# Performance work log

Hardware: AMD Instinct MI355X
Metric: run time of the kernel (lower is better)

The kernel has to match this reference:

```python
import jax, jax.numpy as jnp
import numpy as np

N_HEAD = 16
WINDOW = 256


def setup_inputs() -> dict:
    key = jax.random.key(0)
    ks = jax.random.split(key, 3)
    B, S, D = 2, 2048, 1024
    x = jax.random.normal(ks[0], (B, S, D), dtype=jnp.float32)
    w_attn = jax.random.normal(ks[1], (D, 3 * D), dtype=jnp.float32) * 0.02
    b_attn = jnp.zeros((3 * D,), dtype=jnp.float32)
    w_proj = jax.random.normal(ks[2], (D, D), dtype=jnp.float32) * 0.02
    b_proj = jnp.zeros((D,), dtype=jnp.float32)
    return {"x": x, "w_attn": w_attn, "b_attn": b_attn, "w_proj": w_proj, "b_proj": b_proj}


def reference(x, w_attn, b_attn, w_proj, b_proj):
    B, S, D = x.shape
    hd = D // N_HEAD  # head dim
    scale = 1.0 / np.sqrt(hd).astype(np.float32)

    # fused QKV projection (Conv1D == linear on last dim)
    c = jnp.einsum('bsd,df->bsf', x, w_attn) + b_attn
    q, k, v = jnp.split(c, 3, axis=-1)

    def split_heads(t):  # [B,S,D] -> [B,H,S,hd]
        return t.reshape(B, S, N_HEAD, hd).transpose(0, 2, 1, 3)

    q, k, v = split_heads(q), split_heads(k), split_heads(v)
    present = jnp.stack([k, v], axis=1)  # [B,2,H,S,hd]

    # scores [B,H,S,S]
    w = jnp.einsum('bhqd,bhkd->bhqk', q, k) * scale

    # causal sliding-window mask
    q_pos = jnp.arange(S)[:, None]
    k_pos = jnp.arange(S)[None, :]
    mask = (k_pos <= q_pos) & (k_pos >= q_pos - WINDOW + 1)  # [S,S]
    w = jnp.where(mask[None, None], w, jnp.finfo(w.dtype).min)
    w = jax.nn.softmax(w, axis=-1)

    a = jnp.einsum('bhqk,bhkd->bhqd', w, v)
    a = a.transpose(0, 2, 1, 3).reshape(B, S, D)  # merge heads
    out = jnp.einsum('bsd,df->bsf', a, w_proj) + b_proj
    return out, present
```

## Files before the change

kernel.cpp:

```cpp
#include <hip/hip_runtime.h>
#include <cstdint>
#include <cstddef>

typedef __bf16 bf16x8 __attribute__((ext_vector_type(8)));
typedef float f32x4 __attribute__((ext_vector_type(4)));

#define MFMA16(a, b, c) __builtin_amdgcn_mfma_f32_16x16x32_bf16(a, b, c, 0, 0, 0)

static __device__ __forceinline__ bf16x8 ld_bf16x8(const __bf16* p) {
    return *reinterpret_cast<const bf16x8*>(p);
}

static __device__ __forceinline__ void async_cp16(const __bf16* g, __bf16* l) {
    __builtin_amdgcn_global_load_lds((const __attribute__((address_space(1))) void*)g,
                                     (__attribute__((address_space(3))) void*)l, 16, 0, 0);
}

template <int N>
static __device__ __forceinline__ void wait_vmcnt() {
    asm volatile("s_waitcnt vmcnt(%0)" ::"n"(N) : "memory");
}

static __device__ __forceinline__ void barrier_pinned() {
    __builtin_amdgcn_sched_barrier(0);
    __builtin_amdgcn_s_barrier();
    __builtin_amdgcn_sched_barrier(0);
}

static __device__ __forceinline__ float ex2(float x) {
    return __builtin_amdgcn_exp2f(x);
}

template <int CTRL>
static __device__ __forceinline__ float dppmv(float x) {
    return __builtin_bit_cast(float, __builtin_amdgcn_update_dpp(
        0, __builtin_bit_cast(int, x), CTRL, 0xF, 0xF, true));
}
static __device__ __forceinline__ float rmax16(float x) {
    x = fmaxf(x, dppmv<0x121>(x));
    x = fmaxf(x, dppmv<0x122>(x));
    x = fmaxf(x, dppmv<0x124>(x));
    x = fmaxf(x, dppmv<0x128>(x));
    return x;
}
static __device__ __forceinline__ float rsum16(float x) {
    x += dppmv<0x121>(x);
    x += dppmv<0x122>(x);
    x += dppmv<0x124>(x);
    x += dppmv<0x128>(x);
    return x;
}

__global__ void cvt_kernel(const float* __restrict__ src, __bf16* __restrict__ dst, int n8) {
    int i = blockIdx.x * blockDim.x + threadIdx.x;
    if (i >= n8) return;
    const float4* s4 = reinterpret_cast<const float4*>(src) + (size_t)i * 2;
    float4 a = s4[0], b = s4[1];
    bf16x8 o;
    o[0] = (__bf16)a.x; o[1] = (__bf16)a.y; o[2] = (__bf16)a.z; o[3] = (__bf16)a.w;
    o[4] = (__bf16)b.x; o[5] = (__bf16)b.y; o[6] = (__bf16)b.z; o[7] = (__bf16)b.w;
    reinterpret_cast<bf16x8*>(dst)[i] = o;
}

__global__ __launch_bounds__(256) void tcvt_kernel(const float* __restrict__ in,
                                                   __bf16* __restrict__ out, int K, int N) {
    __shared__ __bf16 T[64][72];
    const int k0 = blockIdx.y * 64, n0 = blockIdx.x * 64;
    const int t = threadIdx.x;
    const int col = (t & 15) << 2;
    const int rowb = t >> 4;
    #pragma unroll
    for (int i = 0; i < 4; i++) {
        int row = i * 16 + rowb;
        float4 v = *reinterpret_cast<const float4*>(&in[(size_t)(k0 + row) * N + n0 + col]);
        T[col + 0][row] = (__bf16)v.x;
        T[col + 1][row] = (__bf16)v.y;
        T[col + 2][row] = (__bf16)v.z;
        T[col + 3][row] = (__bf16)v.w;
    }
    __syncthreads();
    const int oc = (t & 7) << 3;
    const int orb = t >> 3;
    #pragma unroll
    for (int i = 0; i < 2; i++) {
        int r = i * 32 + orb;
        bf16x8 v = *reinterpret_cast<bf16x8*>(&T[r][oc]);
        *reinterpret_cast<bf16x8*>(&out[(size_t)(n0 + r) * K + k0 + oc]) = v;
    }
}

template <int BM, int BN, int WM, int WN>
__device__ __forceinline__ void mainloop2(const __bf16* __restrict__ A,
                                          const __bf16* __restrict__ Bt,
                                          int K, int row0, int col0,
                                          __bf16* lds,
                                          f32x4 (&acc)[BM / WM / 16][BN / WN / 16]) {
    constexpr int MR = BM / WM / 16, NR = BN / WN / 16;
    constexpr int AE = BM * 32;
    constexpr int BUFE = AE + BN * 32;
    constexpr int APW = BM / 16 / 8;
    constexpr int BPW = BN / 16 / 8;
    const int tid = threadIdx.x, l = tid & 63, w = tid >> 6;
    const int wm = w / WN, wn = w % WN;
    const int lr = l >> 2;
    const int lcs = (((l & 3) ^ ((l >> 3) & 3)) << 3);
    const int fr = l & 15;
    const int fc = (((l >> 4) ^ ((l >> 1) & 3)) << 3);

    const size_t arow = (size_t)(row0 + lr) * K + lcs;
    const size_t brow = (size_t)(col0 + lr) * K + lcs;
    const int nt = K >> 5;

    auto stage = [&](int t, int buf) {
        const int k0 = t << 5;
        const int bb = buf * BUFE;
        #pragma unroll
        for (int j = 0; j < APW; j++) {
            const int mi = w * APW + j;
            async_cp16(A + arow + (size_t)mi * 16 * K + k0, lds + bb + mi * 512 + l * 8);
        }
        #pragma unroll
        for (int j = 0; j < BPW; j++) {
            const int ni = w * BPW + j;
            async_cp16(Bt + brow + (size_t)ni * 16 * K + k0, lds + bb + AE + ni * 512 + l * 8);
        }
    };

    stage(0, 0);
    stage(1, 1);

    const int aoff = (wm * (BM / WM) + fr) * 32 + fc;
    const int boff = AE + (wn * (BN / WN) + fr) * 32 + fc;

    int p = 0;
    for (int t = 0; t < nt; ++t) {
        if (t + 1 < nt) {
            wait_vmcnt<APW + BPW>();
        } else {
            wait_vmcnt<0>();
        }
        barrier_pinned();
        if (t + 2 < nt) {
            int p2 = p + 2; if (p2 >= 3) p2 -= 3;
            stage(t + 2, p2);
        }
        const int cb = p * BUFE;
        bf16x8 af[MR], bfv[NR];
        #pragma unroll
        for (int m = 0; m < MR; m++) af[m] = ld_bf16x8(&lds[cb + aoff + m * 512]);
        #pragma unroll
        for (int n = 0; n < NR; n++) bfv[n] = ld_bf16x8(&lds[cb + boff + n * 512]);
        __builtin_amdgcn_s_setprio(1);
        #pragma unroll
        for (int m = 0; m < MR; m++) {
            #pragma unroll
            for (int n = 0; n < NR; n++) {
                acc[m][n] = MFMA16(af[m], bfv[n], acc[m][n]);
            }
        }
        __builtin_amdgcn_s_setprio(0);
        asm volatile("s_waitcnt lgkmcnt(0)" ::: "memory");
        __builtin_amdgcn_sched_barrier(0);
        p = (p == 2) ? 0 : p + 1;
    }
}

__global__ __launch_bounds__(512, 2) void gemm_qkv_kernel(const __bf16* __restrict__ xb,
                                                          const __bf16* __restrict__ wabt,
                                                          const float* __restrict__ bias,
                                                          __bf16* __restrict__ qb,
                                                          __bf16* __restrict__ kb,
                                                          __bf16* __restrict__ vt,
                                                          float* __restrict__ present) {
    __shared__ __bf16 lds[3 * (256 * 32 + 128 * 32)];
    f32x4 acc[4][4] = {};
    const int row0 = blockIdx.y * 256, col0 = blockIdx.x * 128;
    mainloop2<256, 128, 4, 2>(xb, wabt, 1024, row0, col0, lds, acc);

    const int l = threadIdx.x & 63, w = threadIdx.x >> 6;
    const int wm = w >> 1, wn = w & 1;
    const int part = col0 >> 10;
    #pragma unroll
    for (int n = 0; n < 4; n++) {
        int col = col0 + wn * 64 + n * 16 + (l & 15);
        int hh = (col >> 6) & 15;
        int dd = col & 63;
        float bv = bias[col];
        #pragma unroll
        for (int m = 0; m < 4; m++) {
            #pragma unroll
            for (int r = 0; r < 4; r++) {
                int row = row0 + wm * 64 + m * 16 + ((l >> 4) << 2) + r;
                int bb = row >> 11, ss = row & 2047;
                float val = acc[m][n][r] + bv;
                size_t qi = (((size_t)(bb * 16 + hh)) * 2048 + ss) * 64 + dd;
                if (part == 0) {
                    qb[qi] = (__bf16)val;
                } else if (part == 1) {
                    kb[qi] = (__bf16)val;
                    present[(((size_t)((bb * 2 + 0) * 16 + hh)) * 2048 + ss) * 64 + dd] = val;
                } else {
                    vt[(((size_t)(bb * 16 + hh)) * 64 + dd) * 2048 + ss] = (__bf16)val;
                    present[(((size_t)((bb * 2 + 1) * 16 + hh)) * 2048 + ss) * 64 + dd] = val;
                }
            }
        }
    }
}

__global__ __launch_bounds__(512, 2) void gemm_proj_kernel(const __bf16* __restrict__ ab,
                                                           const __bf16* __restrict__ wpbt,
                                                           const float* __restrict__ bias,
                                                           float* __restrict__ out) {
    __shared__ __bf16 lds[3 * (128 * 32 + 128 * 32)];
    f32x4 acc[2][4] = {};
    const int row0 = blockIdx.y * 128, col0 = blockIdx.x * 128;
    mainloop2<128, 128, 4, 2>(ab, wpbt, 1024, row0, col0, lds, acc);

    const int lane = threadIdx.x & 63, w = threadIdx.x >> 6;
    const int wm = w >> 1, wn = w & 1;
    #pragma unroll
    for (int n = 0; n < 4; n++) {
        int col = col0 + wn * 64 + n * 16 + (lane & 15);
        float bv = bias[col];
        #pragma unroll
        for (int m = 0; m < 2; m++) {
            #pragma unroll
            for (int r = 0; r < 4; r++) {
                int row = row0 + wm * 32 + m * 16 + ((lane >> 4) << 2) + r;
                out[(size_t)row * 1024 + col] = acc[m][n][r] + bv;
            }
        }
    }
}

__global__ __launch_bounds__(256) void attn_kernel(const __bf16* __restrict__ qb,
                                                   const __bf16* __restrict__ kb,
                                                   const __bf16* __restrict__ vtb,
                                                   __bf16* __restrict__ ab) {
    __shared__ __bf16 Pls[4][16 * 72];
    const int bidx = blockIdx.x;
    const int xcd = bidx & 7, idx = bidx >> 3;
    const int bh = (xcd << 2) | (idx & 3);
    const int qt = idx >> 2;
    const int lane = threadIdx.x & 63, wid = threadIdx.x >> 6;
    const int q0w = qt * 64 + wid * 16;

    const __bf16* Qh = qb + (size_t)bh * 2048 * 64;
    const __bf16* Kh = kb + (size_t)bh * 2048 * 64;
    const __bf16* Vt = vtb + (size_t)bh * 64 * 2048;
    __bf16* Pw = &Pls[wid][0];

    const int ld16 = lane & 15, hi3 = (lane >> 4) << 3;

    bf16x8 qf[2];
    {
        const __bf16* qp = Qh + (size_t)(q0w + ld16) * 64 + hi3;
        qf[0] = ld_bf16x8(qp);
        qf[1] = ld_bf16x8(qp + 32);
    }

    f32x4 o[4];
    #pragma unroll
    for (int dt = 0; dt < 4; dt++) o[dt] = (f32x4){0.f, 0.f, 0.f, 0.f};
    float mrun[4] = {-1e30f, -1e30f, -1e30f, -1e30f};
    float srun[4] = {0.f, 0.f, 0.f, 0.f};

    const float cl2 = 0.18033688f;
    int klo = q0w - 255;
    int kt0 = klo > 0 ? (klo & ~63) : 0;
    const int ktend = q0w + 15;

    for (int kt = kt0; kt <= ktend; kt += 64) {
        bf16x8 kf[4][2];
        #pragma unroll
        for (int kc = 0; kc < 4; kc++) {
            const __bf16* kp = Kh + (size_t)(kt + kc * 16 + ld16) * 64 + hi3;
            kf[kc][0] = ld_bf16x8(kp);
            kf[kc][1] = ld_bf16x8(kp + 32);
        }
        bf16x8 va[4], vb[4];
        #pragma unroll
        for (int dt = 0; dt < 4; dt++) {
            const __bf16* vp = &Vt[(size_t)(dt * 16 + ld16) * 2048 + kt + hi3];
            va[dt] = ld_bf16x8(vp);
            vb[dt] = ld_bf16x8(vp + 32);
        }
        f32x4 s[4];
        __builtin_amdgcn_s_setprio(1);
        #pragma unroll
        for (int kc = 0; kc < 4; kc++) {
            f32x4 a = (f32x4){0.f, 0.f, 0.f, 0.f};
            a = MFMA16(qf[0], kf[kc][0], a);
            a = MFMA16(qf[1], kf[kc][1], a);
            s[kc] = a;
        }
        __builtin_amdgcn_s_setprio(0);
        const bool clean = (kt >= q0w - 240) && (kt + 63 <= q0w);
        float pv0[4], pv1[4], pv2[4], pv3[4];
        if (clean) {
            float mxs[4];
            #pragma unroll
            for (int r = 0; r < 4; r++) {
                float m = fmaxf(fmaxf(s[0][r], s[1][r]), fmaxf(s[2][r], s[3][r]));
                mxs[r] = rmax16(m) * cl2;
            }
            float grow = fmaxf(fmaxf(mxs[0] - mrun[0], mxs[1] - mrun[1]),
                               fmaxf(mxs[2] - mrun[2], mxs[3] - mrun[3]));
            if (__all(grow <= 8.f)) {
                #pragma unroll
                for (int r = 0; r < 4; r++) {
                    float p0 = ex2(s[0][r] * cl2 - mrun[r]);
                    float p1 = ex2(s[1][r] * cl2 - mrun[r]);
                    float p2 = ex2(s[2][r] * cl2 - mrun[r]);
                    float p3 = ex2(s[3][r] * cl2 - mrun[r]);
                    srun[r] += rsum16((p0 + p1) + (p2 + p3));
                    pv0[r] = p0; pv1[r] = p1; pv2[r] = p2; pv3[r] = p3;
                }
            } else {
                float factor[4];
                #pragma unroll
                for (int r = 0; r < 4; r++) {
                    float mn = fmaxf(mrun[r], mxs[r]);
                    float f = ex2(mrun[r] - mn);
                    float p0 = ex2(s[0][r] * cl2 - mn);
                    float p1 = ex2(s[1][r] * cl2 - mn);
                    float p2 = ex2(s[2][r] * cl2 - mn);
                    float p3 = ex2(s[3][r] * cl2 - mn);
                    srun[r] = srun[r] * f + rsum16((p0 + p1) + (p2 + p3));
                    mrun[r] = mn;
                    factor[r] = f;
                    pv0[r] = p0; pv1[r] = p1; pv2[r] = p2; pv3[r] = p3;
                }
                #pragma unroll
                for (int dt = 0; dt < 4; dt++) {
                    #pragma unroll
                    for (int r = 0; r < 4; r++) o[dt][r] *= factor[r];
                }
            }
        } else {
            float factor[4];
            #pragma unroll
            for (int r = 0; r < 4; r++) {
                int q = q0w + ((lane >> 4) << 2) + r;
                int kb0 = kt + ld16;
                bool ok0 = (kb0 <= q) && (kb0 > q - 256);
                bool ok1 = (kb0 + 16 <= q) && (kb0 + 16 > q - 256);
                bool ok2 = (kb0 + 32 <= q) && (kb0 + 32 > q - 256);
                bool ok3 = (kb0 + 48 <= q) && (kb0 + 48 > q - 256);
                float t0 = ok0 ? s[0][r] * cl2 : -1e30f;
                float t1 = ok1 ? s[1][r] * cl2 : -1e30f;
                float t2 = ok2 ? s[2][r] * cl2 : -1e30f;
                float t3 = ok3 ? s[3][r] * cl2 : -1e30f;
                float mx = rmax16(fmaxf(fmaxf(t0, t1), fmaxf(t2, t3)));
                float mn = fmaxf(mrun[r], mx);
                float f = ex2(mrun[r] - mn);
                float p0 = ok0 ? ex2(t0 - mn) : 0.f;
                float p1 = ok1 ? ex2(t1 - mn) : 0.f;
                float p2 = ok2 ? ex2(t2 - mn) : 0.f;
                float p3 = ok3 ? ex2(t3 - mn) : 0.f;
                srun[r] = srun[r] * f + rsum16((p0 + p1) + (p2 + p3));
                mrun[r] = mn;
                factor[r] = f;
                pv0[r] = p0; pv1[r] = p1; pv2[r] = p2; pv3[r] = p3;
            }
            #pragma unroll
            for (int dt = 0; dt < 4; dt++) {
                #pragma unroll
                for (int r = 0; r < 4; r++) o[dt][r] *= factor[r];
            }
        }
        #pragma unroll
        for (int r = 0; r < 4; r++) {
            int qrow = ((lane >> 4) << 2) + r;
            Pw[qrow * 72 + ld16]      = (__bf16)pv0[r];
            Pw[qrow * 72 + 16 + ld16] = (__bf16)pv1[r];
            Pw[qrow * 72 + 32 + ld16] = (__bf16)pv2[r];
            Pw[qrow * 72 + 48 + ld16] = (__bf16)pv3[r];
        }
        asm volatile("s_waitcnt lgkmcnt(0)" ::: "memory");
        bf16x8 pfA = ld_bf16x8(&Pw[ld16 * 72 + hi3]);
        bf16x8 pfB = ld_bf16x8(&Pw[ld16 * 72 + 32 + hi3]);
        __builtin_amdgcn_s_setprio(1);
        #pragma unroll
        for (int dt = 0; dt < 4; dt++) o[dt] = MFMA16(pfA, va[dt], o[dt]);
        #pragma unroll
        for (int dt = 0; dt < 4; dt++) o[dt] = MFMA16(pfB, vb[dt], o[dt]);
        __builtin_amdgcn_s_setprio(0);
    }

    const int bb = bh >> 4, hh = bh & 15;
    #pragma unroll
    for (int r = 0; r < 4; r++) {
        int q = q0w + ((lane >> 4) << 2) + r;
        float inv = 1.f / srun[r];
        size_t base = ((size_t)bb * 2048 + q) * 1024 + hh * 64;
        #pragma unroll
        for (int dt = 0; dt < 4; dt++) {
            ab[base + dt * 16 + ld16] = (__bf16)(o[dt][r] * inv);
        }
    }
}

extern "C" void kernel_launch(void* const* d_in, const int* in_sizes, int n_in,
                              void* d_out, int out_size, void* d_ws, size_t ws_size,
                              hipStream_t stream) {
    const float* x = (const float*)d_in[0];
    const float* w_attn = (const float*)d_in[1];
    const float* b_attn = (const float*)d_in[2];
    const float* w_proj = (const float*)d_in[3];
    const float* b_proj = (const float*)d_in[4];

    float* out = (float*)d_out;
    float* present = out + (size_t)2 * 2048 * 1024;

    char* w = (char*)d_ws;
    __bf16* xb   = (__bf16*)(w);
    __bf16* wabt = (__bf16*)(w + 8388608);
    __bf16* wpbt = (__bf16*)(w + 14680064);
    __bf16* qb   = (__bf16*)(w + 16777216);
    __bf16* kb   = (__bf16*)(w + 25165824);
    __bf16* vt   = (__bf16*)(w + 33554432);
    __bf16* ab   = xb;

    cvt_kernel<<<2048, 256, 0, stream>>>(x, xb, 524288);
    tcvt_kernel<<<dim3(48, 16), 256, 0, stream>>>(w_attn, wabt, 1024, 3072);
    tcvt_kernel<<<dim3(16, 16), 256, 0, stream>>>(w_proj, wpbt, 1024, 1024);

    gemm_qkv_kernel<<<dim3(24, 16), 512, 0, stream>>>(xb, wabt, b_attn, qb, kb, vt, present);

    attn_kernel<<<1024, 256, 0, stream>>>(qb, kb, vt, ab);

    gemm_proj_kernel<<<dim3(8, 32), 512, 0, stream>>>(ab, wpbt, b_proj, out);
}
```

Baseline: 125.9 us.

## Split attention key range across wave pairs and shrink QKV GEMM row tile

The attention kernel now gives each 16-query tile to two waves that process alternating 64-key blocks. Their partial softmax states are merged through shared memory, so the grid doubles to 2048 blocks and each wave runs fewer serial iterations. The QKV GEMM row tile is halved from 256 to 128, doubling its grid to raise occupancy and CU coverage across the device. The cost is an extra barrier and LDS combine step in attention, plus less operand reuse per GEMM tile.

```diff
diff --git a/kernel.cpp b/kernel.cpp
--- a/kernel.cpp
+++ b/kernel.cpp
@@ -172,10 +172,10 @@
                                                           __bf16* __restrict__ kb,
                                                           __bf16* __restrict__ vt,
                                                           float* __restrict__ present) {
-    __shared__ __bf16 lds[3 * (256 * 32 + 128 * 32)];
-    f32x4 acc[4][4] = {};
-    const int row0 = blockIdx.y * 256, col0 = blockIdx.x * 128;
-    mainloop2<256, 128, 4, 2>(xb, wabt, 1024, row0, col0, lds, acc);
+    __shared__ __bf16 lds[3 * (128 * 32 + 128 * 32)];
+    f32x4 acc[2][4] = {};
+    const int row0 = blockIdx.y * 128, col0 = blockIdx.x * 128;
+    mainloop2<128, 128, 4, 2>(xb, wabt, 1024, row0, col0, lds, acc);
 
     const int l = threadIdx.x & 63, w = threadIdx.x >> 6;
     const int wm = w >> 1, wn = w & 1;
@@ -187,10 +187,10 @@
         int dd = col & 63;
         float bv = bias[col];
         #pragma unroll
-        for (int m = 0; m < 4; m++) {
-            #pragma unroll
-            for (int r = 0; r < 4; r++) {
-                int row = row0 + wm * 64 + m * 16 + ((l >> 4) << 2) + r;
+        for (int m = 0; m < 2; m++) {
+            #pragma unroll
+            for (int r = 0; r < 4; r++) {
+                int row = row0 + wm * 32 + m * 16 + ((l >> 4) << 2) + r;
                 int bb = row >> 11, ss = row & 2047;
                 float val = acc[m][n][r] + bv;
                 size_t qi = (((size_t)(bb * 16 + hh)) * 2048 + ss) * 64 + dd;
@@ -239,19 +239,21 @@
                                                    const __bf16* __restrict__ vtb,
                                                    __bf16* __restrict__ ab) {
     __shared__ __bf16 Pls[4][16 * 72];
+    __shared__ float combsh[2176];
     const int bidx = blockIdx.x;
     const int xcd = bidx & 7, idx = bidx >> 3;
     const int bh = (xcd << 2) | (idx & 3);
     const int qt = idx >> 2;
     const int lane = threadIdx.x & 63, wid = threadIdx.x >> 6;
-    const int q0w = qt * 64 + wid * 16;
+    const int qsub = wid >> 1, half = wid & 1;
+    const int q0w = qt * 32 + qsub * 16;
 
     const __bf16* Qh = qb + (size_t)bh * 2048 * 64;
     const __bf16* Kh = kb + (size_t)bh * 2048 * 64;
     const __bf16* Vt = vtb + (size_t)bh * 64 * 2048;
     __bf16* Pw = &Pls[wid][0];
 
-    const int ld16 = lane & 15, hi3 = (lane >> 4) << 3;
+    const int ld16 = lane & 15, hi3 = (lane >> 4) << 3, hi4 = (lane >> 4) << 2;
 
     bf16x8 qf[2];
     {
@@ -271,7 +273,7 @@
     int kt0 = klo > 0 ? (klo & ~63) : 0;
     const int ktend = q0w + 15;
 
-    for (int kt = kt0; kt <= ktend; kt += 64) {
+    for (int kt = kt0 + half * 64; kt <= ktend; kt += 128) {
         bf16x8 kf[4][2];
         #pragma unroll
         for (int kc = 0; kc < 4; kc++) {
@@ -342,7 +344,7 @@
             float factor[4];
             #pragma unroll
             for (int r = 0; r < 4; r++) {
-                int q = q0w + ((lane >> 4) << 2) + r;
+                int q = q0w + hi4 + r;
                 int kb0 = kt + ld16;
                 bool ok0 = (kb0 <= q) && (kb0 > q - 256);
                 bool ok1 = (kb0 + 16 <= q) && (kb0 + 16 > q - 256);
@@ -372,7 +374,7 @@
         }
         #pragma unroll
         for (int r = 0; r < 4; r++) {
-            int qrow = ((lane >> 4) << 2) + r;
+            int qrow = hi4 + r;
             Pw[qrow * 72 + ld16]      = (__bf16)pv0[r];
             Pw[qrow * 72 + 16 + ld16] = (__bf16)pv1[r];
             Pw[qrow * 72 + 32 + ld16] = (__bf16)pv2[r];
@@ -389,15 +391,45 @@
         __builtin_amdgcn_s_setprio(0);
     }
 
-    const int bb = bh >> 4, hh = bh & 15;
-    #pragma unroll
-    for (int r = 0; r < 4; r++) {
-        int q = q0w + ((lane >> 4) << 2) + r;
-        float inv = 1.f / srun[r];
-        size_t base = ((size_t)bb * 2048 + q) * 1024 + hh * 64;
+    if (half == 1) {
         #pragma unroll
         for (int dt = 0; dt < 4; dt++) {
-            ab[base + dt * 16 + ld16] = (__bf16)(o[dt][r] * inv);
+            #pragma unroll
+            for (int r = 0; r < 4; r++) {
+                combsh[(qsub * 16 + hi4 + r) * 66 + dt * 16 + ld16] = o[dt][r];
+            }
+        }
+        if (ld16 == 0) {
+            #pragma unroll
+            for (int r = 0; r < 4; r++) {
+                combsh[2112 + qsub * 16 + hi4 + r] = mrun[r];
+                combsh[2144 + qsub * 16 + hi4 + r] = srun[r];
+            }
+        }
+    }
+    __syncthreads();
+    if (half == 0) {
+        float f0[4], f1[4];
+        #pragma unroll
+        for (int r = 0; r < 4; r++) {
+            float m1 = combsh[2112 + qsub * 16 + hi4 + r];
+            float s1 = combsh[2144 + qsub * 16 + hi4 + r];
+            float mm = fmaxf(mrun[r], m1);
+            f0[r] = ex2(mrun[r] - mm);
+            f1[r] = ex2(m1 - mm);
+            srun[r] = srun[r] * f0[r] + s1 * f1[r];
+        }
+        const int bb = bh >> 4, hh = bh & 15;
+        #pragma unroll
+        for (int r = 0; r < 4; r++) {
+            int q = q0w + hi4 + r;
+            float inv = 1.f / srun[r];
+            size_t base = ((size_t)bb * 2048 + q) * 1024 + hh * 64;
+            #pragma unroll
+            for (int dt = 0; dt < 4; dt++) {
+                float o1 = combsh[(qsub * 16 + hi4 + r) * 66 + dt * 16 + ld16];
+                ab[base + dt * 16 + ld16] = (__bf16)((o[dt][r] * f0[r] + o1 * f1[r]) * inv);
+            }
         }
     }
 }
@@ -427,9 +459,9 @@
     tcvt_kernel<<<dim3(48, 16), 256, 0, stream>>>(w_attn, wabt, 1024, 3072);
     tcvt_kernel<<<dim3(16, 16), 256, 0, stream>>>(w_proj, wpbt, 1024, 1024);
 
-    gemm_qkv_kernel<<<dim3(24, 16), 512, 0, stream>>>(xb, wabt, b_attn, qb, kb, vt, present);
-
-    attn_kernel<<<1024, 256, 0, stream>>>(qb, kb, vt, ab);
+    gemm_qkv_kernel<<<dim3(24, 32), 512, 0, stream>>>(xb, wabt, b_attn, qb, kb, vt, present);
+
+    attn_kernel<<<2048, 256, 0, stream>>>(qb, kb, vt, ab);
 
     gemm_proj_kernel<<<dim3(8, 32), 512, 0, stream>>>(ab, wpbt, b_proj, out);
 }
```

Result: faster. 120.0 us (-4.7%).

## Use two-pass softmax with LDS-staged K tiles and smaller QKV GEMM tiles

Applied to the files above, without the earlier changes.

The attention kernel now stages every K tile the block needs into swizzled LDS with async copies, then runs two passes. The first pass computes QK^T to find the exact row max. The second recomputes the scores and exponentiates against that fixed max, which removes online-softmax rescaling, per-tile cross-lane reductions and branches, at the cost of doing the QK MFMAs twice. The QKV GEMM tile shrinks from 256x128 to 128x128 and the grid doubles, giving more blocks for better CU coverage. The attention kernel also gets an occupancy hint of 3 blocks per CU.

```diff
diff --git a/kernel.cpp b/kernel.cpp
--- a/kernel.cpp
+++ b/kernel.cpp
@@ -172,10 +172,10 @@
                                                           __bf16* __restrict__ kb,
                                                           __bf16* __restrict__ vt,
                                                           float* __restrict__ present) {
-    __shared__ __bf16 lds[3 * (256 * 32 + 128 * 32)];
-    f32x4 acc[4][4] = {};
-    const int row0 = blockIdx.y * 256, col0 = blockIdx.x * 128;
-    mainloop2<256, 128, 4, 2>(xb, wabt, 1024, row0, col0, lds, acc);
+    __shared__ __bf16 lds[3 * (128 * 32 + 128 * 32)];
+    f32x4 acc[2][4] = {};
+    const int row0 = blockIdx.y * 128, col0 = blockIdx.x * 128;
+    mainloop2<128, 128, 4, 2>(xb, wabt, 1024, row0, col0, lds, acc);
 
     const int l = threadIdx.x & 63, w = threadIdx.x >> 6;
     const int wm = w >> 1, wn = w & 1;
@@ -187,10 +187,10 @@
         int dd = col & 63;
         float bv = bias[col];
         #pragma unroll
-        for (int m = 0; m < 4; m++) {
+        for (int m = 0; m < 2; m++) {
             #pragma unroll
             for (int r = 0; r < 4; r++) {
-                int row = row0 + wm * 64 + m * 16 + ((l >> 4) << 2) + r;
+                int row = row0 + wm * 32 + m * 16 + ((l >> 4) << 2) + r;
                 int bb = row >> 11, ss = row & 2047;
                 float val = acc[m][n][r] + bv;
                 size_t qi = (((size_t)(bb * 16 + hh)) * 2048 + ss) * 64 + dd;
@@ -234,24 +234,38 @@
     }
 }
 
-__global__ __launch_bounds__(256) void attn_kernel(const __bf16* __restrict__ qb,
-                                                   const __bf16* __restrict__ kb,
-                                                   const __bf16* __restrict__ vtb,
-                                                   __bf16* __restrict__ ab) {
+__global__ __launch_bounds__(256, 3) void attn_kernel(const __bf16* __restrict__ qb,
+                                                      const __bf16* __restrict__ kb,
+                                                      const __bf16* __restrict__ vtb,
+                                                      __bf16* __restrict__ ab) {
+    __shared__ __bf16 Kls[5 * 4096];
     __shared__ __bf16 Pls[4][16 * 72];
     const int bidx = blockIdx.x;
     const int xcd = bidx & 7, idx = bidx >> 3;
     const int bh = (xcd << 2) | (idx & 3);
-    const int qt = idx >> 2;
+    const int qc = idx >> 2;
     const int lane = threadIdx.x & 63, wid = threadIdx.x >> 6;
-    const int q0w = qt * 64 + wid * 16;
+    const int q0blk = qc * 64;
+    const int q0w = q0blk + wid * 16;
 
     const __bf16* Qh = qb + (size_t)bh * 2048 * 64;
     const __bf16* Kh = kb + (size_t)bh * 2048 * 64;
     const __bf16* Vt = vtb + (size_t)bh * 64 * 2048;
     __bf16* Pw = &Pls[wid][0];
 
-    const int ld16 = lane & 15, hi3 = (lane >> 4) << 3;
+    const int ld16 = lane & 15, hi3 = (lane >> 4) << 3, hi4 = (lane >> 4) << 2;
+
+    int tmp = q0blk - 255;
+    const int kt0 = tmp > 0 ? (tmp & ~63) : 0;
+    const int NT = ((q0blk + 63 - kt0) >> 6) + 1;
+
+    const int sswz = (((lane & 7) ^ (lane >> 3)) << 3);
+    for (int j = wid; j < NT * 8; j += 4) {
+        const int tj = j >> 3, c = j & 7;
+        const int kt = kt0 + tj * 64;
+        const __bf16* src = Kh + (size_t)(kt + c * 8 + (lane >> 3)) * 64 + sswz;
+        async_cp16(src, &Kls[j * 512 + lane * 8]);
+    }
 
     bf16x8 qf[2];
     {
@@ -259,26 +273,62 @@
         qf[0] = ld_bf16x8(qp);
         qf[1] = ld_bf16x8(qp + 32);
     }
+    wait_vmcnt<0>();
+    __syncthreads();
+
+    const float cl2 = 0.18033688f;
+    const int rdswz = (lane & 7) << 3;
+
+    auto qks = [&](int t, int kt, f32x4 (&s)[4]) {
+        const __bf16* tb = &Kls[t * 4096];
+        #pragma unroll
+        for (int kc = 0; kc < 4; kc++) {
+            const int rbase = (kc * 16 + ld16) * 64;
+            bf16x8 k0 = ld_bf16x8(&tb[rbase + ((hi3) ^ rdswz)]);
+            bf16x8 k1 = ld_bf16x8(&tb[rbase + ((32 + hi3) ^ rdswz)]);
+            f32x4 a = (f32x4){0.f, 0.f, 0.f, 0.f};
+            a = MFMA16(qf[0], k0, a);
+            a = MFMA16(qf[1], k1, a);
+            s[kc] = a;
+        }
+        const bool clean = (kt >= q0w - 240) && (kt + 63 <= q0w);
+        if (!clean) {
+            #pragma unroll
+            for (int r = 0; r < 4; r++) {
+                int q = q0w + hi4 + r;
+                #pragma unroll
+                for (int kc = 0; kc < 4; kc++) {
+                    int ki = kt + kc * 16 + ld16;
+                    bool ok = (ki <= q) && (ki > q - 256);
+                    s[kc][r] = ok ? s[kc][r] : -1e30f;
+                }
+            }
+        }
+    };
+
+    float mr[4] = {-1e30f, -1e30f, -1e30f, -1e30f};
+    for (int t = 0; t < NT; t++) {
+        const int kt = kt0 + t * 64;
+        if (kt + 63 < q0w - 255 || kt > q0w + 15) continue;
+        f32x4 s[4];
+        qks(t, kt, s);
+        #pragma unroll
+        for (int r = 0; r < 4; r++) {
+            mr[r] = fmaxf(mr[r], fmaxf(fmaxf(s[0][r], s[1][r]), fmaxf(s[2][r], s[3][r])));
+        }
+    }
+    float m2[4];
+    #pragma unroll
+    for (int r = 0; r < 4; r++) m2[r] = rmax16(mr[r]) * cl2;
 
     f32x4 o[4];
     #pragma unroll
     for (int dt = 0; dt < 4; dt++) o[dt] = (f32x4){0.f, 0.f, 0.f, 0.f};
-    float mrun[4] = {-1e30f, -1e30f, -1e30f, -1e30f};
-    float srun[4] = {0.f, 0.f, 0.f, 0.f};
-
-    const float cl2 = 0.18033688f;
-    int klo = q0w - 255;
-    int kt0 = klo > 0 ? (klo & ~63) : 0;
-    const int ktend = q0w + 15;
-
-    for (int kt = kt0; kt <= ktend; kt += 64) {
-        bf16x8 kf[4][2];
-        #pragma unroll
-        for (int kc = 0; kc < 4; kc++) {
-            const __bf16* kp = Kh + (size_t)(kt + kc * 16 + ld16) * 64 + hi3;
-            kf[kc][0] = ld_bf16x8(kp);
-            kf[kc][1] = ld_bf16x8(kp + 32);
-        }
+    float sl[4] = {0.f, 0.f, 0.f, 0.f};
+
+    for (int t = 0; t < NT; t++) {
+        const int kt = kt0 + t * 64;
+        if (kt + 63 < q0w - 255 || kt > q0w + 15) continue;
         bf16x8 va[4], vb[4];
         #pragma unroll
         for (int dt = 0; dt < 4; dt++) {
@@ -287,96 +337,19 @@
             vb[dt] = ld_bf16x8(vp + 32);
         }
         f32x4 s[4];
-        __builtin_amdgcn_s_setprio(1);
-        #pragma unroll
-        for (int kc = 0; kc < 4; kc++) {
-            f32x4 a = (f32x4){0.f, 0.f, 0.f, 0.f};
-            a = MFMA16(qf[0], kf[kc][0], a);
-            a = MFMA16(qf[1], kf[kc][1], a);
-            s[kc] = a;
-        }
-        __builtin_amdgcn_s_setprio(0);
-        const bool clean = (kt >= q0w - 240) && (kt + 63 <= q0w);
-        float pv0[4], pv1[4], pv2[4], pv3[4];
-        if (clean) {
-            float mxs[4];
-            #pragma unroll
-            for (int r = 0; r < 4; r++) {
-                float m = fmaxf(fmaxf(s[0][r], s[1][r]), fmaxf(s[2][r], s[3][r]));
-                mxs[r] = rmax16(m) * cl2;
-            }
-            float grow = fmaxf(fmaxf(mxs[0] - mrun[0], mxs[1] - mrun[1]),
-                               fmaxf(mxs[2] - mrun[2], mxs[3] - mrun[3]));
-            if (__all(grow <= 8.f)) {
-                #pragma unroll
-                for (int r = 0; r < 4; r++) {
-                    float p0 = ex2(s[0][r] * cl2 - mrun[r]);
-                    float p1 = ex2(s[1][r] * cl2 - mrun[r]);
-                    float p2 = ex2(s[2][r] * cl2 - mrun[r]);
-                    float p3 = ex2(s[3][r] * cl2 - mrun[r]);
-                    srun[r] += rsum16((p0 + p1) + (p2 + p3));
-                    pv0[r] = p0; pv1[r] = p1; pv2[r] = p2; pv3[r] = p3;
-                }
-            } else {
-                float factor[4];
-                #pragma unroll
-                for (int r = 0; r < 4; r++) {
-                    float mn = fmaxf(mrun[r], mxs[r]);
-                    float f = ex2(mrun[r] - mn);
-                    float p0 = ex2(s[0][r] * cl2 - mn);
-                    float p1 = ex2(s[1][r] * cl2 - mn);
-                    float p2 = ex2(s[2][r] * cl2 - mn);
-                    float p3 = ex2(s[3][r] * cl2 - mn);
-                    srun[r] = srun[r] * f + rsum16((p0 + p1) + (p2 + p3));
-                    mrun[r] = mn;
-                    factor[r] = f;
-                    pv0[r] = p0; pv1[r] = p1; pv2[r] = p2; pv3[r] = p3;
-                }
-                #pragma unroll
-                for (int dt = 0; dt < 4; dt++) {
-                    #pragma unroll
-                    for (int r = 0; r < 4; r++) o[dt][r] *= factor[r];
-                }
-            }
-        } else {
-            float factor[4];
-            #pragma unroll
-            for (int r = 0; r < 4; r++) {
-                int q = q0w + ((lane >> 4) << 2) + r;
-                int kb0 = kt + ld16;
-                bool ok0 = (kb0 <= q) && (kb0 > q - 256);
-                bool ok1 = (kb0 + 16 <= q) && (kb0 + 16 > q - 256);
-                bool ok2 = (kb0 + 32 <= q) && (kb0 + 32 > q - 256);
-                bool ok3 = (kb0 + 48 <= q) && (kb0 + 48 > q - 256);
-                float t0 = ok0 ? s[0][r] * cl2 : -1e30f;
-                float t1 = ok1 ? s[1][r] * cl2 : -1e30f;
-                float t2 = ok2 ? s[2][r] * cl2 : -1e30f;
-                float t3 = ok3 ? s[3][r] * cl2 : -1e30f;
-                float mx = rmax16(fmaxf(fmaxf(t0, t1), fmaxf(t2, t3)));
-                float mn = fmaxf(mrun[r], mx);
-                float f = ex2(mrun[r] - mn);
-                float p0 = ok0 ? ex2(t0 - mn) : 0.f;
-                float p1 = ok1 ? ex2(t1 - mn) : 0.f;
-                float p2 = ok2 ? ex2(t2 - mn) : 0.f;
-                float p3 = ok3 ? ex2(t3 - mn) : 0.f;
-                srun[r] = srun[r] * f + rsum16((p0 + p1) + (p2 + p3));
-                mrun[r] = mn;
-                factor[r] = f;
-                pv0[r] = p0; pv1[r] = p1; pv2[r] = p2; pv3[r] = p3;
-            }
-            #pragma unroll
-            for (int dt = 0; dt < 4; dt++) {
-                #pragma unroll
-                for (int r = 0; r < 4; r++) o[dt][r] *= factor[r];
-            }
-        }
+        qks(t, kt, s);
         #pragma unroll
         for (int r = 0; r < 4; r++) {
-            int qrow = ((lane >> 4) << 2) + r;
-            Pw[qrow * 72 + ld16]      = (__bf16)pv0[r];
-            Pw[qrow * 72 + 16 + ld16] = (__bf16)pv1[r];
-            Pw[qrow * 72 + 32 + ld16] = (__bf16)pv2[r];
-            Pw[qrow * 72 + 48 + ld16] = (__bf16)pv3[r];
+            float p0 = ex2(fmaf(s[0][r], cl2, -m2[r]));
+            float p1 = ex2(fmaf(s[1][r], cl2, -m2[r]));
+            float p2 = ex2(fmaf(s[2][r], cl2, -m2[r]));
+            float p3 = ex2(fmaf(s[3][r], cl2, -m2[r]));
+            sl[r] += (p0 + p1) + (p2 + p3);
+            int qrow = hi4 + r;
+            Pw[qrow * 72 + ld16]      = (__bf16)p0;
+            Pw[qrow * 72 + 16 + ld16] = (__bf16)p1;
+            Pw[qrow * 72 + 32 + ld16] = (__bf16)p2;
+            Pw[qrow * 72 + 48 + ld16] = (__bf16)p3;
         }
         asm volatile("s_waitcnt lgkmcnt(0)" ::: "memory");
         bf16x8 pfA = ld_bf16x8(&Pw[ld16 * 72 + hi3]);
@@ -392,8 +365,8 @@
     const int bb = bh >> 4, hh = bh & 15;
     #pragma unroll
     for (int r = 0; r < 4; r++) {
-        int q = q0w + ((lane >> 4) << 2) + r;
-        float inv = 1.f / srun[r];
+        float inv = 1.f / rsum16(sl[r]);
+        int q = q0w + hi4 + r;
         size_t base = ((size_t)bb * 2048 + q) * 1024 + hh * 64;
         #pragma unroll
         for (int dt = 0; dt < 4; dt++) {
@@ -427,7 +400,7 @@
     tcvt_kernel<<<dim3(48, 16), 256, 0, stream>>>(w_attn, wabt, 1024, 3072);
     tcvt_kernel<<<dim3(16, 16), 256, 0, stream>>>(w_proj, wpbt, 1024, 1024);
 
-    gemm_qkv_kernel<<<dim3(24, 16), 512, 0, stream>>>(xb, wabt, b_attn, qb, kb, vt, present);
+    gemm_qkv_kernel<<<dim3(24, 32), 512, 0, stream>>>(xb, wabt, b_attn, qb, kb, vt, present);
 
     attn_kernel<<<1024, 256, 0, stream>>>(qb, kb, vt, ab);
 
```

After: 107.4 us. 1.17x faster.
